# Performance work log

Hardware: AMD Instinct MI355X
Metric: run time of the kernel (lower is better)

Reference implementation:

```python
import jax, jax.numpy as jnp
import numpy as np

NUM_HEADS = 8
HEAD_SPLITS = (2, 3, 3)      # heads per CRPE window (CoaT default {3:2,5:3,7:3})
KERNELS = (3, 5, 7)
DIM = 256
CH = DIM // NUM_HEADS        # 32
N_DET = 100


def setup_inputs() -> dict:
    key = jax.random.key(0)
    ks = jax.random.split(key, 12)
    B, Hs, Ws, C = 4, 128, 128, DIM
    N = Hs * Ws
    inp = {
        "x": jax.random.normal(ks[0], (B, N, C), dtype=jnp.float32),
        "det": jax.random.normal(ks[1], (B, N_DET, C), dtype=jnp.float32),
        "H": Hs,
        "W": Ws,
        # qkv Linear (dim -> 3*dim, bias=True); stored as [in, out] for x @ W
        "qkv_w": jax.random.normal(ks[2], (C, 3 * C), dtype=jnp.float32) * 0.02,
        "qkv_b": jnp.zeros((3 * C,), dtype=jnp.float32),
        # output proj Linear (dim -> dim)
        "proj_w": jax.random.normal(ks[3], (C, C), dtype=jnp.float32) * 0.02,
        "proj_b": jnp.zeros((C,), dtype=jnp.float32),
    }
    # CRPE depthwise conv weights: per window k, channels = head_split * CH
    for i, (hs, k) in enumerate(zip(HEAD_SPLITS, KERNELS)):
        ch = hs * CH
        inp[f"crpe_w{k}"] = jax.random.normal(ks[4 + i], (ch, 1, k, k), dtype=jnp.float32) * 0.05
        inp[f"crpe_b{k}"] = jnp.zeros((ch,), dtype=jnp.float32)
    return inp


def _crpe(q, v, H, W, crpe_w3, crpe_b3, crpe_w5, crpe_b5, crpe_w7, crpe_b7):
    # q, v: [B, h, N, Ch], N == H*W  (CoaT ConvRelPosEnc)
    B, h, N, Ch = q.shape
    v_img = jnp.transpose(v, (0, 1, 3, 2)).reshape(B, h * Ch, H, W)
    splits = np.cumsum([hs * Ch for hs in HEAD_SPLITS])[:-1]
    parts = jnp.split(v_img, splits, axis=1)
    ws = (crpe_w3, crpe_w5, crpe_w7)
    bs = (crpe_b3, crpe_b5, crpe_b7)
    outs = []
    for part, w, b, k in zip(parts, ws, bs, KERNELS):
        pad = k // 2
        o = jax.lax.conv_general_dilated(
            part, w, window_strides=(1, 1), padding=[(pad, pad), (pad, pad)],
            feature_group_count=part.shape[1],  # depthwise
            dimension_numbers=("NCHW", "OIHW", "NCHW"))
        outs.append(o + b[None, :, None, None])
    conv_v = jnp.concatenate(outs, axis=1).reshape(B, h, Ch, N)
    conv_v = jnp.transpose(conv_v, (0, 1, 3, 2))  # [B,h,N,Ch]
    return q * conv_v


def reference(x, det, H, W, qkv_w, qkv_b, proj_w, proj_b,
              crpe_w3, crpe_b3, crpe_w5, crpe_b5, crpe_w7, crpe_b7):
    B, N, C = x.shape
    h = NUM_HEADS
    Ch = C // h
    scale = Ch ** (-0.5)

    xcat = jnp.concatenate([x, det], axis=1)          # [B, N+M, C]
    full_qkv = xcat @ qkv_w + qkv_b                   # [B, N+M, 3C]

    # ---- patch branch: factorized (linear) attention + CRPE ----
    patch_qkv = full_qkv[:, :N, :].reshape(B, N, 3, h, Ch)
    patch_qkv = jnp.transpose(patch_qkv, (2, 0, 3, 1, 4))  # [3,B,h,N,Ch]
    pq, pk, pv = patch_qkv[0], patch_qkv[1], patch_qkv[2]
    k_softmax = jax.nn.softmax(pk, axis=2)                 # softmax over tokens
    factor = jnp.einsum('bhnc,bhnd->bhcd', k_softmax, pv)  # [B,h,Ch,Ch]
    factor_att = jnp.einsum('bhnc,bhcd->bhnd', pq, factor) # [B,h,N,Ch]
    crpe = _crpe(pq, pv, H, W, crpe_w3, crpe_b3, crpe_w5, crpe_b5, crpe_w7, crpe_b7)
    patch_x = scale * factor_att + crpe
    patch_x = jnp.transpose(patch_x, (0, 2, 1, 3)).reshape(B, N, C)

    # ---- det branch: standard softmax self-attention ----
    det_qkv = full_qkv[:, N:, :].reshape(B, -1, 3, h, Ch)
    det_qkv = jnp.transpose(det_qkv, (2, 0, 3, 1, 4))      # [3,B,h,M,Ch]
    dq, dk, dv = det_qkv[0], det_qkv[1], det_qkv[2]
    attn = jax.nn.softmax((dq * scale) @ jnp.swapaxes(dk, -2, -1), axis=-1)
    det_x = jnp.transpose(attn @ dv, (0, 2, 1, 3)).reshape(B, -1, C)

    out = jnp.concatenate([patch_x, det_x], axis=1) @ proj_w + proj_b
    return out[:, :N, :], out[:, N:, :]
```

## Files before the change

### kernel.cpp

```cpp
#include <hip/hip_runtime.h>

#define NHEADS 8
#define CHD 32
#define CDIM 256
#define C3 768
#define NTOK 16384
#define MDET 100
#define TPB (NTOK + MDET)
#define BATCH 4
#define ROWS (BATCH * TPB)
#define HH 128
#define WW 128
#define SCALE 0.17677669529663687f
#define SCH 32
#define FCH 16

typedef unsigned short u16;
typedef __attribute__((ext_vector_type(8))) __bf16 bf16x8;
typedef __attribute__((ext_vector_type(4))) float f32x4;

__device__ __forceinline__ float bf2f(u16 u) {
  union { unsigned int i; float f; } z; z.i = ((unsigned int)u) << 16; return z.f;
}
__device__ __forceinline__ u16 f2bf(float f) {
  __bf16 h = (__bf16)f;
  return __builtin_bit_cast(unsigned short, h);
}

static const size_t B_QX     = 0;
static const size_t B_KVB    = B_QX + (size_t)ROWS * 256 * 2;
static const size_t B_WQT    = B_KVB + (size_t)ROWS * 512 * 2;
static const size_t B_WPT    = B_WQT + (size_t)768 * 256 * 2;
static const size_t B_PM     = B_WPT + (size_t)256 * 256 * 2;
static const size_t B_PS     = B_PM + 1024 * 32 * 4;
static const size_t B_FPART  = B_PS + 1024 * 32 * 4;
static const size_t B_FACTOR = B_FPART + (size_t)512 * 1024 * 4;
static const size_t B_LSE    = B_FACTOR + 32768 * 4;
static const size_t B_END    = B_LSE + 1024 * 4;

__global__ __launch_bounds__(256)
void wconv(const float* __restrict__ qkv_w, const float* __restrict__ proj_w,
           u16* __restrict__ WqT, u16* __restrict__ WpT) {
  int o = blockIdx.x * 256 + threadIdx.x;
  if (o < 768 * 256) {
    int n = o >> 8, k = o & 255;
    WqT[o] = f2bf(qkv_w[(size_t)k * C3 + n]);
  } else {
    int p = o - 768 * 256;
    int n = p >> 8, k = p & 255;
    WpT[p] = f2bf(proj_w[(size_t)k * CDIM + n]);
  }
}

__global__ __launch_bounds__(256)
void gemm_qkv(const float* __restrict__ x, const float* __restrict__ det,
              const u16* __restrict__ WqT, const float* __restrict__ bias,
              u16* __restrict__ qx, u16* __restrict__ kv) {
  const int row0 = blockIdx.x * 128;
  const int col0 = blockIdx.y * 128;
  const int tid = threadIdx.x;
  const int lane = tid & 63;
  const int wid = tid >> 6;
  const int wm = (wid & 1) * 64;
  const int wn = (wid >> 1) * 64;
  const int m16 = lane & 15;
  const int kg8 = (lane >> 4) * 8;

  __shared__ u16 As[128][72];
  __shared__ u16 Bs[128][72];

  const int sr = tid >> 1;
  const int sk = (tid & 1) * 32;

  int grow = row0 + sr;
  int crow = grow < ROWS ? grow : ROWS - 1;
  int bb = crow / TPB, tt = crow - bb * TPB;
  const float* aptr = (tt < NTOK)
      ? x + (size_t)(bb * NTOK + tt) * CDIM
      : det + (size_t)(bb * MDET + (tt - NTOK)) * CDIM;
  const u16* bptr = WqT + (size_t)(col0 + sr) * CDIM;

  f32x4 acc[4][4];
#pragma unroll
  for (int ni = 0; ni < 4; ++ni) {
    float bv = bias[col0 + wn + ni * 16 + m16];
#pragma unroll
    for (int mi = 0; mi < 4; ++mi)
      acc[mi][ni] = (f32x4){bv, bv, bv, bv};
  }

  for (int k0 = 0; k0 < CDIM; k0 += 64) {
#pragma unroll
    for (int j = 0; j < 4; ++j) {
      float4 v0 = *(const float4*)(aptr + k0 + sk + j * 8);
      float4 v1 = *(const float4*)(aptr + k0 + sk + j * 8 + 4);
      ushort4 u0, u1;
      u0.x = f2bf(v0.x); u0.y = f2bf(v0.y); u0.z = f2bf(v0.z); u0.w = f2bf(v0.w);
      u1.x = f2bf(v1.x); u1.y = f2bf(v1.y); u1.z = f2bf(v1.z); u1.w = f2bf(v1.w);
      *(ushort4*)&As[sr][sk + j * 8] = u0;
      *(ushort4*)&As[sr][sk + j * 8 + 4] = u1;
      *(uint4*)&Bs[sr][sk + j * 8] = *(const uint4*)(bptr + k0 + sk + j * 8);
    }
    __syncthreads();
#pragma unroll
    for (int kk = 0; kk < 2; ++kk) {
      bf16x8 af[4], bfr[4];
#pragma unroll
      for (int mi = 0; mi < 4; ++mi)
        af[mi] = *(const bf16x8*)&As[wm + mi * 16 + m16][kk * 32 + kg8];
#pragma unroll
      for (int ni = 0; ni < 4; ++ni)
        bfr[ni] = *(const bf16x8*)&Bs[wn + ni * 16 + m16][kk * 32 + kg8];
#pragma unroll
      for (int mi = 0; mi < 4; ++mi)
#pragma unroll
        for (int ni = 0; ni < 4; ++ni)
          acc[mi][ni] = __builtin_amdgcn_mfma_f32_16x16x32_bf16(
              af[mi], bfr[ni], acc[mi][ni], 0, 0, 0);
    }
    __syncthreads();
  }

  u16* obase; int ostride, ocol0;
  if (col0 < 256) { obase = qx; ostride = 256; ocol0 = col0; }
  else            { obase = kv; ostride = 512; ocol0 = col0 - 256; }
  const int rbase = (lane >> 4) * 4;
#pragma unroll
  for (int mi = 0; mi < 4; ++mi) {
#pragma unroll
    for (int ni = 0; ni < 4; ++ni) {
      int col = ocol0 + wn + ni * 16 + m16;
#pragma unroll
      for (int r = 0; r < 4; ++r) {
        int rr = row0 + wm + mi * 16 + rbase + r;
        if (rr < ROWS)
          obase[(size_t)rr * ostride + col] = f2bf(acc[mi][ni][r]);
      }
    }
  }
}

__global__ __launch_bounds__(256)
void gemm_proj(const u16* __restrict__ xin, const u16* __restrict__ WpT,
               const float* __restrict__ bias, float* __restrict__ dout) {
  const int row0 = blockIdx.x * 128;
  const int col0 = blockIdx.y * 128;
  const int tid = threadIdx.x;
  const int lane = tid & 63;
  const int wid = tid >> 6;
  const int wm = (wid & 1) * 64;
  const int wn = (wid >> 1) * 64;
  const int m16 = lane & 15;
  const int kg8 = (lane >> 4) * 8;

  __shared__ u16 As[128][72];
  __shared__ u16 Bs[128][72];

  const int sr = tid >> 1;
  const int sk = (tid & 1) * 32;

  int grow = row0 + sr;
  int crow = grow < ROWS ? grow : ROWS - 1;
  const u16* aptr = xin + (size_t)crow * CDIM;
  const u16* bptr = WpT + (size_t)(col0 + sr) * CDIM;

  f32x4 acc[4][4];
#pragma unroll
  for (int ni = 0; ni < 4; ++ni) {
    float bv = bias[col0 + wn + ni * 16 + m16];
#pragma unroll
    for (int mi = 0; mi < 4; ++mi)
      acc[mi][ni] = (f32x4){bv, bv, bv, bv};
  }

  for (int k0 = 0; k0 < CDIM; k0 += 64) {
#pragma unroll
    for (int j = 0; j < 4; ++j) {
      *(uint4*)&As[sr][sk + j * 8] = *(const uint4*)(aptr + k0 + sk + j * 8);
      *(uint4*)&Bs[sr][sk + j * 8] = *(const uint4*)(bptr + k0 + sk + j * 8);
    }
    __syncthreads();
#pragma unroll
    for (int kk = 0; kk < 2; ++kk) {
      bf16x8 af[4], bfr[4];
#pragma unroll
      for (int mi = 0; mi < 4; ++mi)
        af[mi] = *(const bf16x8*)&As[wm + mi * 16 + m16][kk * 32 + kg8];
#pragma unroll
      for (int ni = 0; ni < 4; ++ni)
        bfr[ni] = *(const bf16x8*)&Bs[wn + ni * 16 + m16][kk * 32 + kg8];
#pragma unroll
      for (int mi = 0; mi < 4; ++mi)
#pragma unroll
        for (int ni = 0; ni < 4; ++ni)
          acc[mi][ni] = __builtin_amdgcn_mfma_f32_16x16x32_bf16(
              af[mi], bfr[ni], acc[mi][ni], 0, 0, 0);
    }
    __syncthreads();
  }

  const int rbase = (lane >> 4) * 4;
#pragma unroll
  for (int mi = 0; mi < 4; ++mi) {
#pragma unroll
    for (int r = 0; r < 4; ++r) {
      int rr = row0 + wm + mi * 16 + rbase + r;
      if (rr >= ROWS) continue;
      int b = rr / TPB, t = rr - b * TPB;
      float* dst = (t < NTOK)
          ? dout + ((size_t)b * NTOK + t) * CDIM
          : dout + (size_t)BATCH * NTOK * CDIM + ((size_t)b * MDET + (t - NTOK)) * CDIM;
#pragma unroll
      for (int ni = 0; ni < 4; ++ni)
        dst[col0 + wn + ni * 16 + m16] = acc[mi][ni][r];
    }
  }
}

__global__ __launch_bounds__(256)
void kstats(const u16* __restrict__ kv, float* __restrict__ pm,
            float* __restrict__ ps) {
  const int bid = blockIdx.x;
  const int chunk = bid & (SCH - 1);
  const int h = (bid / SCH) & 7;
  const int b = bid / (SCH * 8);
  const int tid = threadIdx.x;
  const int c = tid & 31, sub = tid >> 5;
  const size_t base = (size_t)b * TPB * 512 + h * CHD + c;
  const int t0 = chunk * (NTOK / SCH);
  float m = -1e30f, s = 0.f;
  for (int i = sub; i < NTOK / SCH; i += 8) {
    float k = bf2f(kv[base + (size_t)(t0 + i) * 512]);
    float nm = fmaxf(m, k);
    s = s * __expf(m - nm) + __expf(k - nm);
    m = nm;
  }
  __shared__ float sm[8][32], ss[8][32];
  sm[sub][c] = m; ss[sub][c] = s;
  __syncthreads();
  if (sub == 0) {
    for (int j = 1; j < 8; ++j) {
      float m2 = sm[j][c], s2 = ss[j][c];
      float nm = fmaxf(m, m2);
      s = s * __expf(m - nm) + s2 * __expf(m2 - nm);
      m = nm;
    }
    pm[bid * 32 + c] = m;
    ps[bid * 32 + c] = s;
  }
}

__global__ void kmerge(const float* __restrict__ pm, const float* __restrict__ ps,
                       float* __restrict__ lse) {
  int g = blockIdx.x * blockDim.x + threadIdx.x;
  if (g >= BATCH * 8 * 32) return;
  int c = g & 31, bh = g >> 5;
  float m = -1e30f, s = 0.f;
  for (int ch = 0; ch < SCH; ++ch) {
    int bid = bh * SCH + ch;
    float m2 = pm[bid * 32 + c], s2 = ps[bid * 32 + c];
    float nm = fmaxf(m, m2);
    s = s * __expf(m - nm) + s2 * __expf(m2 - nm);
    m = nm;
  }
  lse[g] = m + logf(s);
}

__global__ __launch_bounds__(256)
void kfactor(const u16* __restrict__ kv, const float* __restrict__ lse,
             float* __restrict__ fpart) {
  const int bid = blockIdx.x;
  const int chunk = bid & (FCH - 1);
  const int h = (bid / FCH) & 7;
  const int b = bid / (FCH * 8);
  const int tid = threadIdx.x;
  const int c = tid & 31;
  const int d0 = (tid >> 5) * 4;
  const float lse_c = lse[(b * 8 + h) * 32 + c];
  __shared__ float wsm[64][32];
  __shared__ float vsm[64][33];
  float a0 = 0.f, a1 = 0.f, a2 = 0.f, a3 = 0.f;
  const int t0 = chunk * (NTOK / FCH);
  const size_t rowb = (size_t)b * TPB;
  for (int st = 0; st < (NTOK / FCH) / 64; ++st) {
    int tb = t0 + st * 64;
#pragma unroll
    for (int i = 0; i < 8; ++i) {
      int flat = tid + i * 256;
      int tt = flat >> 5;
      int cc = flat & 31;
      size_t a = (rowb + tb + tt) * (size_t)512 + h * CHD + cc;
      wsm[tt][cc] = __expf(bf2f(kv[a]) - lse_c);
      vsm[tt][cc] = bf2f(kv[a + 256]);
    }
    __syncthreads();
#pragma unroll 4
    for (int tt = 0; tt < 64; ++tt) {
      float w = wsm[tt][c];
      a0 += w * vsm[tt][d0 + 0];
      a1 += w * vsm[tt][d0 + 1];
      a2 += w * vsm[tt][d0 + 2];
      a3 += w * vsm[tt][d0 + 3];
    }
    __syncthreads();
  }
  float* fp = fpart + ((size_t)bid * 32 + c) * 32 + d0;
  fp[0] = a0; fp[1] = a1; fp[2] = a2; fp[3] = a3;
}

__global__ void fmerge(const float* __restrict__ fpart, float* __restrict__ factor) {
  int o = blockIdx.x * 256 + threadIdx.x;
  if (o >= BATCH * 8 * CHD * CHD) return;
  int cd = o & 1023, bh = o >> 10;
  float s = 0.f;
  for (int ch = 0; ch < FCH; ++ch)
    s += fpart[((size_t)(bh * FCH + ch) << 10) + cd];
  factor[o] = s;
}

template <int K>
__device__ __forceinline__ void conv_tail(
    const float* __restrict__ wp, float wb,
    const u16 (&vt)[22][22][32], const u16 (&qt)[256][32],
    const float (&freg)[32], int c, int pg, size_t obase,
    u16* __restrict__ xo) {
  float w[K * K];
#pragma unroll
  for (int i = 0; i < K * K; ++i) w[i] = wp[i];
  for (int i = 0; i < 32; ++i) {
    const int pos = pg * 32 + i;
    const int sy = pos >> 4, sx = pos & 15;
    float fa = 0.f;
#pragma unroll
    for (int cc = 0; cc < 32; ++cc) fa += bf2f(qt[pos][cc]) * freg[cc];
    float o = wb;
#pragma unroll
    for (int dy = 0; dy < K; ++dy)
#pragma unroll
      for (int dx = 0; dx < K; ++dx)
        o += w[dy * K + dx] * bf2f(vt[sy + 3 + dy - K / 2][sx + 3 + dx - K / 2][c]);
    const float res = SCALE * fa + bf2f(qt[pos][c]) * o;
    xo[obase + (size_t)((sy << 7) + sx) * CDIM] = f2bf(res);
  }
}

__global__ __launch_bounds__(256)
void kpatch2(const u16* __restrict__ qx, const u16* __restrict__ kv,
             const float* __restrict__ factor,
             const float* __restrict__ w3, const float* __restrict__ b3,
             const float* __restrict__ w5, const float* __restrict__ b5,
             const float* __restrict__ w7, const float* __restrict__ b7,
             u16* __restrict__ xout) {
  const int bid = blockIdx.x;
  const int b = bid >> 9;
  const int h = (bid >> 6) & 7;
  const int tile = bid & 63;
  const int y0 = (tile >> 3) * 16, x0 = (tile & 7) * 16;
  const int tid = threadIdx.x;

  __shared__ u16 vt[22][22][32];
  __shared__ u16 qt[256][32];
  __shared__ float fsm[32][32];

  const size_t tokbase = (size_t)b * TPB;
  for (int idx = tid; idx < 22 * 22 * 4; idx += 256) {
    int pos = idx >> 2, c8 = (idx & 3) * 8;
    int py = pos / 22, px = pos - py * 22;
    int y = y0 + py - 3, x = x0 + px - 3;
    uint4 v = make_uint4(0u, 0u, 0u, 0u);
    if (y >= 0 && y < HH && x >= 0 && x < WW)
      v = *(const uint4*)(kv + (tokbase + (y << 7) + x) * 512 + 256 + h * CHD + c8);
    *(uint4*)&vt[py][px][c8] = v;
  }
  for (int idx = tid; idx < 256 * 4; idx += 256) {
    int pos = idx >> 2, c8 = (idx & 3) * 8;
    int y = y0 + (pos >> 4), x = x0 + (pos & 15);
    *(uint4*)&qt[pos][c8] =
        *(const uint4*)(qx + (tokbase + (y << 7) + x) * CDIM + h * CHD + c8);
  }
  for (int idx = tid; idx < 1024; idx += 256)
    fsm[idx >> 5][idx & 31] = factor[(size_t)((b * 8 + h) << 10) + idx];
  __syncthreads();

  const int c = tid & 31;
  const int pg = tid >> 5;
  float freg[32];
#pragma unroll
  for (int cc = 0; cc < 32; ++cc) freg[cc] = fsm[cc][c];

  const size_t obase = (tokbase + (y0 << 7) + x0) * CDIM + h * CHD + c;
  if (h < 2)
    conv_tail<3>(w3 + (h * 32 + c) * 9, b3[h * 32 + c], vt, qt, freg, c, pg, obase, xout);
  else if (h < 5)
    conv_tail<5>(w5 + ((h - 2) * 32 + c) * 25, b5[(h - 2) * 32 + c], vt, qt, freg, c, pg, obase, xout);
  else
    conv_tail<7>(w7 + ((h - 5) * 32 + c) * 49, b7[(h - 5) * 32 + c], vt, qt, freg, c, pg, obase, xout);
}

__global__ __launch_bounds__(128)
void kdet(const u16* __restrict__ qx, const u16* __restrict__ kv,
          u16* __restrict__ xout) {
  const int bid = blockIdx.x;
  const int b = bid >> 3, h = bid & 7;
  const int tid = threadIdx.x;
  __shared__ float qd[100][32], kd[100][32], vd[100][32];
  __shared__ float pd[100][101];
  const size_t rq = ((size_t)b * TPB + NTOK) * CDIM;
  const size_t rk = ((size_t)b * TPB + NTOK) * 512;
  for (int flat = tid; flat < 100 * 32; flat += 128) {
    int t = flat >> 5, cc = flat & 31;
    qd[t][cc] = bf2f(qx[rq + (size_t)t * CDIM + h * CHD + cc]);
    kd[t][cc] = bf2f(kv[rk + (size_t)t * 512 + h * CHD + cc]);
    vd[t][cc] = bf2f(kv[rk + (size_t)t * 512 + 256 + h * CHD + cc]);
  }
  __syncthreads();
  const int r = tid;
  if (r < 100) {
    float mx = -1e30f;
    for (int j = 0; j < 100; ++j) {
      float s = 0.f;
#pragma unroll
      for (int cc = 0; cc < 32; ++cc) s += qd[r][cc] * kd[j][cc];
      s *= SCALE;
      pd[r][j] = s;
      mx = fmaxf(mx, s);
    }
    float sum = 0.f;
    for (int j = 0; j < 100; ++j) {
      float e = __expf(pd[r][j] - mx);
      pd[r][j] = e;
      sum += e;
    }
    float inv = 1.f / sum;
    for (int d = 0; d < 32; ++d) {
      float o = 0.f;
      for (int j = 0; j < 100; ++j) o += pd[r][j] * vd[j][d];
      xout[rq + (size_t)r * CDIM + h * CHD + d] = f2bf(o * inv);
    }
  }
}

extern "C" void kernel_launch(void* const* d_in, const int* in_sizes, int n_in,
                              void* d_out, int out_size, void* d_ws, size_t ws_size,
                              hipStream_t stream) {
  if (ws_size < B_END) return;

  const float* x      = (const float*)d_in[0];
  const float* det    = (const float*)d_in[1];
  const float* qkv_w  = (const float*)d_in[4];
  const float* qkv_b  = (const float*)d_in[5];
  const float* proj_w = (const float*)d_in[6];
  const float* proj_b = (const float*)d_in[7];
  const float* w3     = (const float*)d_in[8];
  const float* b3     = (const float*)d_in[9];
  const float* w5     = (const float*)d_in[10];
  const float* b5     = (const float*)d_in[11];
  const float* w7     = (const float*)d_in[12];
  const float* b7     = (const float*)d_in[13];

  char* wsb = (char*)d_ws;
  u16* qx      = (u16*)(wsb + B_QX);
  u16* kv      = (u16*)(wsb + B_KVB);
  u16* WqT     = (u16*)(wsb + B_WQT);
  u16* WpT     = (u16*)(wsb + B_WPT);
  float* pm    = (float*)(wsb + B_PM);
  float* ps    = (float*)(wsb + B_PS);
  float* fpart = (float*)(wsb + B_FPART);
  float* factor= (float*)(wsb + B_FACTOR);
  float* lse   = (float*)(wsb + B_LSE);
  float* out   = (float*)d_out;

  wconv<<<1024, 256, 0, stream>>>(qkv_w, proj_w, WqT, WpT);

  dim3 g1((ROWS + 127) / 128, C3 / 128);
  gemm_qkv<<<g1, 256, 0, stream>>>(x, det, WqT, qkv_b, qx, kv);

  kstats<<<BATCH * 8 * SCH, 256, 0, stream>>>(kv, pm, ps);
  kmerge<<<4, 256, 0, stream>>>(pm, ps, lse);
  kfactor<<<BATCH * 8 * FCH, 256, 0, stream>>>(kv, lse, fpart);
  fmerge<<<128, 256, 0, stream>>>(fpart, factor);

  kpatch2<<<BATCH * 8 * 64, 256, 0, stream>>>(qx, kv, factor,
                                              w3, b3, w5, b5, w7, b7, qx);
  kdet<<<BATCH * 8, 128, 0, stream>>>(qx, kv, qx);

  dim3 g2((ROWS + 127) / 128, CDIM / 128);
  gemm_proj<<<g2, 256, 0, stream>>>(qx, WpT, proj_b, out);
}
```

Baseline: 515.9 us.

## Store K/V head-planar, split CRPE patch kernel per window with MFMA factor

The QKV GEMM now writes K and V into separate head-planar buffers, [b,h,token,32], with V stored as fp16. The goal is contiguous per-head reads in the stats, factor, det and patch kernels. The patch kernel is split into three templated launches, one per conv kernel size, so each launch drops the per-block branch. Inside it, q·factor runs on MFMA instead of scalar dot products, and V tiles sit channel-major in shared memory so each thread register-blocks a 16-wide row of depthwise conv outputs. In exchange there are more launches, scattered 2-byte stores in the GEMM epilogue, and the factor_att intermediate is rounded to bf16.

```diff
diff --git a/kernel.cpp b/kernel.cpp
--- a/kernel.cpp
+++ b/kernel.cpp
@@ -1,4 +1,5 @@
 #include <hip/hip_runtime.h>
+#include <hip/hip_fp16.h>
 
 #define NHEADS 8
 #define CHD 32
@@ -28,8 +29,9 @@
 }
 
 static const size_t B_QX     = 0;
-static const size_t B_KVB    = B_QX + (size_t)ROWS * 256 * 2;
-static const size_t B_WQT    = B_KVB + (size_t)ROWS * 512 * 2;
+static const size_t B_KPL    = B_QX + (size_t)ROWS * 256 * 2;
+static const size_t B_VPL    = B_KPL + (size_t)ROWS * 256 * 2;
+static const size_t B_WQT    = B_VPL + (size_t)ROWS * 256 * 2;
 static const size_t B_WPT    = B_WQT + (size_t)768 * 256 * 2;
 static const size_t B_PM     = B_WPT + (size_t)256 * 256 * 2;
 static const size_t B_PS     = B_PM + 1024 * 32 * 4;
@@ -55,7 +57,7 @@
 __global__ __launch_bounds__(256)
 void gemm_qkv(const float* __restrict__ x, const float* __restrict__ det,
               const u16* __restrict__ WqT, const float* __restrict__ bias,
-              u16* __restrict__ qx, u16* __restrict__ kv) {
+              u16* __restrict__ qx, u16* __restrict__ kpl, __half* __restrict__ vpl) {
   const int row0 = blockIdx.x * 128;
   const int col0 = blockIdx.y * 128;
   const int tid = threadIdx.x;
@@ -121,20 +123,27 @@
     __syncthreads();
   }
 
-  u16* obase; int ostride, ocol0;
-  if (col0 < 256) { obase = qx; ostride = 256; ocol0 = col0; }
-  else            { obase = kv; ostride = 512; ocol0 = col0 - 256; }
   const int rbase = (lane >> 4) * 4;
 #pragma unroll
   for (int mi = 0; mi < 4; ++mi) {
 #pragma unroll
-    for (int ni = 0; ni < 4; ++ni) {
-      int col = ocol0 + wn + ni * 16 + m16;
-#pragma unroll
-      for (int r = 0; r < 4; ++r) {
-        int rr = row0 + wm + mi * 16 + rbase + r;
-        if (rr < ROWS)
-          obase[(size_t)rr * ostride + col] = f2bf(acc[mi][ni][r]);
+    for (int r = 0; r < 4; ++r) {
+      int rr = row0 + wm + mi * 16 + rbase + r;
+      if (rr >= ROWS) continue;
+      int b = rr / TPB, t = rr - b * TPB;
+#pragma unroll
+      for (int ni = 0; ni < 4; ++ni) {
+        int col = col0 + wn + ni * 16 + m16;
+        float v = acc[mi][ni][r];
+        if (col < 256) {
+          qx[(size_t)rr * 256 + col] = f2bf(v);
+        } else if (col < 512) {
+          int cc = col - 256;
+          kpl[((size_t)(b * 8 + (cc >> 5)) * TPB + t) * 32 + (cc & 31)] = f2bf(v);
+        } else {
+          int cc = col - 512;
+          vpl[((size_t)(b * 8 + (cc >> 5)) * TPB + t) * 32 + (cc & 31)] = __float2half(v);
+        }
       }
     }
   }
@@ -218,7 +227,7 @@
 }
 
 __global__ __launch_bounds__(256)
-void kstats(const u16* __restrict__ kv, float* __restrict__ pm,
+void kstats(const u16* __restrict__ kpl, float* __restrict__ pm,
             float* __restrict__ ps) {
   const int bid = blockIdx.x;
   const int chunk = bid & (SCH - 1);
@@ -226,11 +235,11 @@
   const int b = bid / (SCH * 8);
   const int tid = threadIdx.x;
   const int c = tid & 31, sub = tid >> 5;
-  const size_t base = (size_t)b * TPB * 512 + h * CHD + c;
+  const size_t base = ((size_t)(b * 8 + h) * TPB) * 32 + c;
   const int t0 = chunk * (NTOK / SCH);
   float m = -1e30f, s = 0.f;
   for (int i = sub; i < NTOK / SCH; i += 8) {
-    float k = bf2f(kv[base + (size_t)(t0 + i) * 512]);
+    float k = bf2f(kpl[base + (size_t)(t0 + i) * 32]);
     float nm = fmaxf(m, k);
     s = s * __expf(m - nm) + __expf(k - nm);
     m = nm;
@@ -267,8 +276,8 @@
 }
 
 __global__ __launch_bounds__(256)
-void kfactor(const u16* __restrict__ kv, const float* __restrict__ lse,
-             float* __restrict__ fpart) {
+void kfactor(const u16* __restrict__ kpl, const __half* __restrict__ vpl,
+             const float* __restrict__ lse, float* __restrict__ fpart) {
   const int bid = blockIdx.x;
   const int chunk = bid & (FCH - 1);
   const int h = (bid / FCH) & 7;
@@ -281,17 +290,16 @@
   __shared__ float vsm[64][33];
   float a0 = 0.f, a1 = 0.f, a2 = 0.f, a3 = 0.f;
   const int t0 = chunk * (NTOK / FCH);
-  const size_t rowb = (size_t)b * TPB;
   for (int st = 0; st < (NTOK / FCH) / 64; ++st) {
     int tb = t0 + st * 64;
+    const size_t base = ((size_t)(b * 8 + h) * TPB + tb) * 32;
 #pragma unroll
     for (int i = 0; i < 8; ++i) {
       int flat = tid + i * 256;
       int tt = flat >> 5;
       int cc = flat & 31;
-      size_t a = (rowb + tb + tt) * (size_t)512 + h * CHD + cc;
-      wsm[tt][cc] = __expf(bf2f(kv[a]) - lse_c);
-      vsm[tt][cc] = bf2f(kv[a + 256]);
+      wsm[tt][cc] = __expf(bf2f(kpl[base + flat]) - lse_c);
+      vsm[tt][cc] = __half2float(vpl[base + flat]);
     }
     __syncthreads();
 #pragma unroll 4
@@ -319,99 +327,158 @@
 }
 
 template <int K>
-__device__ __forceinline__ void conv_tail(
-    const float* __restrict__ wp, float wb,
-    const u16 (&vt)[22][22][32], const u16 (&qt)[256][32],
-    const float (&freg)[32], int c, int pg, size_t obase,
-    u16* __restrict__ xo) {
-  float w[K * K];
-#pragma unroll
-  for (int i = 0; i < K * K; ++i) w[i] = wp[i];
-  for (int i = 0; i < 32; ++i) {
-    const int pos = pg * 32 + i;
-    const int sy = pos >> 4, sx = pos & 15;
-    float fa = 0.f;
-#pragma unroll
-    for (int cc = 0; cc < 32; ++cc) fa += bf2f(qt[pos][cc]) * freg[cc];
-    float o = wb;
-#pragma unroll
-    for (int dy = 0; dy < K; ++dy)
-#pragma unroll
-      for (int dx = 0; dx < K; ++dx)
-        o += w[dy * K + dx] * bf2f(vt[sy + 3 + dy - K / 2][sx + 3 + dx - K / 2][c]);
-    const float res = SCALE * fa + bf2f(qt[pos][c]) * o;
-    xo[obase + (size_t)((sy << 7) + sx) * CDIM] = f2bf(res);
-  }
-}
-
 __global__ __launch_bounds__(256)
-void kpatch2(const u16* __restrict__ qx, const u16* __restrict__ kv,
+void kpatch3(const u16* __restrict__ qx, const __half* __restrict__ vpl,
              const float* __restrict__ factor,
-             const float* __restrict__ w3, const float* __restrict__ b3,
-             const float* __restrict__ w5, const float* __restrict__ b5,
-             const float* __restrict__ w7, const float* __restrict__ b7,
-             u16* __restrict__ xout) {
+             const float* __restrict__ wk, const float* __restrict__ bk,
+             int h_base, int nh, u16* __restrict__ xout) {
+  constexpr int HE = 16 + K - 1;
+  constexpr int PADK = K / 2;
+  constexpr int CSTRIDE = HE * 24 + 8;
+
+  __shared__ u16 vt[32 * CSTRIDE];
+  __shared__ u16 fa_s[256 * 32];
+  __shared__ u16 FT[32 * 32];
+
   const int bid = blockIdx.x;
-  const int b = bid >> 9;
-  const int h = (bid >> 6) & 7;
   const int tile = bid & 63;
+  const int rem = bid >> 6;
+  const int h = h_base + (rem % nh);
+  const int b = rem / nh;
   const int y0 = (tile >> 3) * 16, x0 = (tile & 7) * 16;
   const int tid = threadIdx.x;
-
-  __shared__ u16 vt[22][22][32];
-  __shared__ u16 qt[256][32];
-  __shared__ float fsm[32][32];
-
-  const size_t tokbase = (size_t)b * TPB;
-  for (int idx = tid; idx < 22 * 22 * 4; idx += 256) {
-    int pos = idx >> 2, c8 = (idx & 3) * 8;
-    int py = pos / 22, px = pos - py * 22;
-    int y = y0 + py - 3, x = x0 + px - 3;
-    uint4 v = make_uint4(0u, 0u, 0u, 0u);
-    if (y >= 0 && y < HH && x >= 0 && x < WW)
-      v = *(const uint4*)(kv + (tokbase + (y << 7) + x) * 512 + 256 + h * CHD + c8);
-    *(uint4*)&vt[py][px][c8] = v;
-  }
-  for (int idx = tid; idx < 256 * 4; idx += 256) {
-    int pos = idx >> 2, c8 = (idx & 3) * 8;
-    int y = y0 + (pos >> 4), x = x0 + (pos & 15);
-    *(uint4*)&qt[pos][c8] =
-        *(const uint4*)(qx + (tokbase + (y << 7) + x) * CDIM + h * CHD + c8);
-  }
-  for (int idx = tid; idx < 1024; idx += 256)
-    fsm[idx >> 5][idx & 31] = factor[(size_t)((b * 8 + h) << 10) + idx];
+  const int btok = b * TPB;
+  const size_t vbase = (size_t)(b * 8 + h) * TPB * 32;
+
+  for (int flat = tid; flat < HE * HE * 8; flat += 256) {
+    int pos = flat >> 3, c4 = (flat & 7) * 4;
+    int y = pos / HE, xx_ = pos - y * HE;
+    int yy = y0 + y - PADK, xx = x0 + xx_ - PADK;
+    ushort4 v = make_ushort4(0, 0, 0, 0);
+    if (yy >= 0 && yy < HH && xx >= 0 && xx < WW)
+      v = *(const ushort4*)((const u16*)vpl + vbase + (size_t)(yy * WW + xx) * 32 + c4);
+    vt[(c4 + 0) * CSTRIDE + y * 24 + xx_] = v.x;
+    vt[(c4 + 1) * CSTRIDE + y * 24 + xx_] = v.y;
+    vt[(c4 + 2) * CSTRIDE + y * 24 + xx_] = v.z;
+    vt[(c4 + 3) * CSTRIDE + y * 24 + xx_] = v.w;
+  }
+  {
+    int flat = tid;
+    int d = flat >> 5, cc = flat & 31;
+    FT[d * 32 + cc] = f2bf(factor[(size_t)((b * 8 + h) << 10) + cc * 32 + d]);
+    flat = tid + 256; d = flat >> 5; cc = flat & 31;
+    FT[d * 32 + cc] = f2bf(factor[(size_t)((b * 8 + h) << 10) + cc * 32 + d]);
+    flat = tid + 512; d = flat >> 5; cc = flat & 31;
+    FT[d * 32 + cc] = f2bf(factor[(size_t)((b * 8 + h) << 10) + cc * 32 + d]);
+    flat = tid + 768; d = flat >> 5; cc = flat & 31;
+    FT[d * 32 + cc] = f2bf(factor[(size_t)((b * 8 + h) << 10) + cc * 32 + d]);
+  }
   __syncthreads();
 
+  {
+    const int lane = tid & 63;
+    const int wid = tid >> 6;
+    const int m16 = lane & 15;
+    const int kg8 = (lane >> 4) * 8;
+    bf16x8 bfr[2];
+#pragma unroll
+    for (int ni = 0; ni < 2; ++ni)
+      bfr[ni] = *(const bf16x8*)&FT[(ni * 16 + m16) * 32 + kg8];
+    f32x4 acc[4][2];
+#pragma unroll
+    for (int mi = 0; mi < 4; ++mi)
+#pragma unroll
+      for (int ni = 0; ni < 2; ++ni)
+        acc[mi][ni] = (f32x4){0.f, 0.f, 0.f, 0.f};
+#pragma unroll
+    for (int mi = 0; mi < 4; ++mi) {
+      int pos = wid * 64 + mi * 16 + m16;
+      int token = (y0 + (pos >> 4)) * 128 + x0 + (pos & 15);
+      bf16x8 af = *(const bf16x8*)(qx + (size_t)(btok + token) * 256 + h * 32 + kg8);
+#pragma unroll
+      for (int ni = 0; ni < 2; ++ni)
+        acc[mi][ni] = __builtin_amdgcn_mfma_f32_16x16x32_bf16(
+            af, bfr[ni], acc[mi][ni], 0, 0, 0);
+    }
+#pragma unroll
+    for (int mi = 0; mi < 4; ++mi)
+#pragma unroll
+      for (int ni = 0; ni < 2; ++ni)
+#pragma unroll
+        for (int r = 0; r < 4; ++r) {
+          int pos = wid * 64 + mi * 16 + (lane >> 4) * 4 + r;
+          fa_s[pos * 32 + ni * 16 + m16] = f2bf(acc[mi][ni][r]);
+        }
+  }
+  __syncthreads();
+
   const int c = tid & 31;
-  const int pg = tid >> 5;
-  float freg[32];
-#pragma unroll
-  for (int cc = 0; cc < 32; ++cc) freg[cc] = fsm[cc][c];
-
-  const size_t obase = (tokbase + (y0 << 7) + x0) * CDIM + h * CHD + c;
-  if (h < 2)
-    conv_tail<3>(w3 + (h * 32 + c) * 9, b3[h * 32 + c], vt, qt, freg, c, pg, obase, xout);
-  else if (h < 5)
-    conv_tail<5>(w5 + ((h - 2) * 32 + c) * 25, b5[(h - 2) * 32 + c], vt, qt, freg, c, pg, obase, xout);
-  else
-    conv_tail<7>(w7 + ((h - 5) * 32 + c) * 49, b7[(h - 5) * 32 + c], vt, qt, freg, c, pg, obase, xout);
+  const int syg = tid >> 5;
+  const int widx = (h - h_base) * 32 + c;
+  float wreg[K * K];
+#pragma unroll
+  for (int i = 0; i < K * K; ++i) wreg[i] = wk[widx * K * K + i];
+  const float wb = bk[widx];
+
+  float o[2][16];
+#pragma unroll
+  for (int ri = 0; ri < 2; ++ri)
+#pragma unroll
+    for (int p = 0; p < 16; ++p) o[ri][p] = 0.f;
+
+#pragma unroll
+  for (int ri = 0; ri < 2; ++ri) {
+    const int yy = syg + ri * 8;
+#pragma unroll
+    for (int dy = 0; dy < K; ++dy) {
+      const int vrow = yy + dy;
+      union { uint4 q[3]; __half hh[24]; } row;
+      row.q[0] = *(const uint4*)&vt[c * CSTRIDE + vrow * 24 + 0];
+      row.q[1] = *(const uint4*)&vt[c * CSTRIDE + vrow * 24 + 8];
+      row.q[2] = *(const uint4*)&vt[c * CSTRIDE + vrow * 24 + 16];
+      float frow[HE];
+#pragma unroll
+      for (int j = 0; j < HE; ++j) frow[j] = __half2float(row.hh[j]);
+#pragma unroll
+      for (int dx = 0; dx < K; ++dx) {
+        const float wv = wreg[dy * K + dx];
+#pragma unroll
+        for (int p = 0; p < 16; ++p)
+          o[ri][p] += wv * frow[p + dx];
+      }
+    }
+  }
+
+#pragma unroll
+  for (int ri = 0; ri < 2; ++ri) {
+    const int yy = syg + ri * 8;
+#pragma unroll
+    for (int p = 0; p < 16; ++p) {
+      const int pos = yy * 16 + p;
+      const int token = (y0 + yy) * 128 + x0 + p;
+      const size_t gidx = (size_t)(btok + token) * 256 + h * 32 + c;
+      float fa = bf2f(fa_s[pos * 32 + c]);
+      float qv = bf2f(qx[gidx]);
+      xout[gidx] = f2bf(SCALE * fa + qv * (o[ri][p] + wb));
+    }
+  }
 }
 
 __global__ __launch_bounds__(128)
-void kdet(const u16* __restrict__ qx, const u16* __restrict__ kv,
-          u16* __restrict__ xout) {
+void kdet(const u16* __restrict__ qx, const u16* __restrict__ kpl,
+          const __half* __restrict__ vpl, u16* __restrict__ xout) {
   const int bid = blockIdx.x;
   const int b = bid >> 3, h = bid & 7;
   const int tid = threadIdx.x;
   __shared__ float qd[100][32], kd[100][32], vd[100][32];
   __shared__ float pd[100][101];
   const size_t rq = ((size_t)b * TPB + NTOK) * CDIM;
-  const size_t rk = ((size_t)b * TPB + NTOK) * 512;
+  const size_t rp = ((size_t)(b * 8 + h) * TPB + NTOK) * 32;
   for (int flat = tid; flat < 100 * 32; flat += 128) {
     int t = flat >> 5, cc = flat & 31;
     qd[t][cc] = bf2f(qx[rq + (size_t)t * CDIM + h * CHD + cc]);
-    kd[t][cc] = bf2f(kv[rk + (size_t)t * 512 + h * CHD + cc]);
-    vd[t][cc] = bf2f(kv[rk + (size_t)t * 512 + 256 + h * CHD + cc]);
+    kd[t][cc] = bf2f(kpl[rp + (size_t)t * 32 + cc]);
+    vd[t][cc] = __half2float(vpl[rp + (size_t)t * 32 + cc]);
   }
   __syncthreads();
   const int r = tid;
@@ -460,7 +527,8 @@
 
   char* wsb = (char*)d_ws;
   u16* qx      = (u16*)(wsb + B_QX);
-  u16* kv      = (u16*)(wsb + B_KVB);
+  u16* kpl     = (u16*)(wsb + B_KPL);
+  __half* vpl  = (__half*)(wsb + B_VPL);
   u16* WqT     = (u16*)(wsb + B_WQT);
   u16* WpT     = (u16*)(wsb + B_WPT);
   float* pm    = (float*)(wsb + B_PM);
@@ -473,16 +541,18 @@
   wconv<<<1024, 256, 0, stream>>>(qkv_w, proj_w, WqT, WpT);
 
   dim3 g1((ROWS + 127) / 128, C3 / 128);
-  gemm_qkv<<<g1, 256, 0, stream>>>(x, det, WqT, qkv_b, qx, kv);
-
-  kstats<<<BATCH * 8 * SCH, 256, 0, stream>>>(kv, pm, ps);
+  gemm_qkv<<<g1, 256, 0, stream>>>(x, det, WqT, qkv_b, qx, kpl, vpl);
+
+  kstats<<<BATCH * 8 * SCH, 256, 0, stream>>>(kpl, pm, ps);
   kmerge<<<4, 256, 0, stream>>>(pm, ps, lse);
-  kfactor<<<BATCH * 8 * FCH, 256, 0, stream>>>(kv, lse, fpart);
+  kfactor<<<BATCH * 8 * FCH, 256, 0, stream>>>(kpl, vpl, lse, fpart);
   fmerge<<<128, 256, 0, stream>>>(fpart, factor);
 
-  kpatch2<<<BATCH * 8 * 64, 256, 0, stream>>>(qx, kv, factor,
-                                              w3, b3, w5, b5, w7, b7, qx);
-  kdet<<<BATCH * 8, 128, 0, stream>>>(qx, kv, qx);
+  kpatch3<3><<<BATCH * 2 * 64, 256, 0, stream>>>(qx, vpl, factor, w3, b3, 0, 2, qx);
+  kpatch3<5><<<BATCH * 3 * 64, 256, 0, stream>>>(qx, vpl, factor, w5, b5, 2, 3, qx);
+  kpatch3<7><<<BATCH * 3 * 64, 256, 0, stream>>>(qx, vpl, factor, w7, b7, 5, 3, qx);
+
+  kdet<<<BATCH * 8, 128, 0, stream>>>(qx, kpl, vpl, qx);
 
   dim3 g2((ROWS + 127) / 128, CDIM / 128);
   gemm_proj<<<g2, 256, 0, stream>>>(qx, WpT, proj_b, out);
```

After: 442.7 us. 1.17x faster.
